# Performance work log

Hardware: AMD Instinct MI355X
Metric: run time of the kernel (lower is better)

## Reference

```python
import jax, jax.numpy as jnp
import numpy as np
import math

THETA = 10000.0

def apply_rope(x, start_pos=0):
    # x: [B, H, S, D], rotate-half RoPE
    B, H, S, D = x.shape
    pos = jnp.arange(start_pos, start_pos + S, dtype=jnp.float32)
    inv_freq = 1.0 / (THETA ** (jnp.arange(0, D, 2, dtype=jnp.float32) / D))  # [D/2]
    ang = pos[:, None] * inv_freq[None, :]  # [S, D/2]
    cos, sin = jnp.cos(ang), jnp.sin(ang)
    x1, x2 = jnp.split(x, 2, axis=-1)
    return jnp.concatenate([x1 * cos - x2 * sin, x1 * sin + x2 * cos], axis=-1)


def setup_inputs() -> dict:
    key = jax.random.key(0)
    ks = jax.random.split(key, 9)
    B, S, E, H, D = 2, 2048, 2048, 16, 128
    s = 0.02
    return {
        "x": jax.random.normal(ks[0], (B, S, E), jnp.float32),
        "W_q": jax.random.normal(ks[1], (E, H * D), jnp.float32) * s,
        "b_q": jnp.zeros((H * D,), jnp.float32),
        "W_k": jax.random.normal(ks[2], (E, D), jnp.float32) * s,
        "b_k": jnp.zeros((D,), jnp.float32),
        "W_v": jax.random.normal(ks[3], (E, D), jnp.float32) * s,
        "b_v": jnp.zeros((D,), jnp.float32),
        "W_o": jax.random.normal(ks[4], (H * D, E), jnp.float32) * s,
        "b_o": jnp.zeros((E,), jnp.float32),
    }


def reference(x, W_q, b_q, W_k, b_k, W_v, b_v, W_o, b_o):
    B, S, E = x.shape
    D = W_k.shape[1]
    H = W_q.shape[1] // D
    # projections (weights stored [in, out])
    q = (x @ W_q + b_q).reshape(B, S, H, D).transpose(0, 2, 1, 3)   # [B,H,S,D]
    k = (x @ W_k + b_k).reshape(B, S, 1, D).transpose(0, 2, 1, 3)   # [B,1,S,D]
    v = (x @ W_v + b_v).reshape(B, S, 1, D).transpose(0, 2, 1, 3)   # [B,1,S,D]
    # RoPE (cache is None -> start_pos = 0)
    q = apply_rope(q, 0)
    k = apply_rope(k, 0)
    # shared-KV attention: k head dim broadcasts over H q heads
    scores = jnp.einsum("bhqd,bokd->bhqk", q, k) / math.sqrt(D)     # [B,H,S,S]
    causal = jnp.tril(jnp.ones((S, S), dtype=bool))
    scores = jnp.where(causal, scores, -jnp.inf)
    attn = jax.nn.softmax(scores, axis=-1)
    out = jnp.einsum("bhqk,bokd->bhqd", attn, v)                    # [B,H,S,D]
    out = out.transpose(0, 2, 1, 3).reshape(B, S, H * D)
    out = out @ W_o + b_o                                           # dropout is identity in eval
    return out
```

## Files before the change

### kernel.cpp

```cpp
#include <hip/hip_runtime.h>
#include <stdint.h>

typedef __bf16 bf16x8 __attribute__((ext_vector_type(8)));
typedef __bf16 bf16x2 __attribute__((ext_vector_type(2)));
typedef float  f32x4  __attribute__((ext_vector_type(4)));
typedef short  s16x8  __attribute__((ext_vector_type(8)));

__device__ inline unsigned short f2b(float f) {
  unsigned int u = __builtin_bit_cast(unsigned int, f);
  u += 0x7FFFu + ((u >> 16) & 1u);
  return (unsigned short)(u >> 16);
}
__device__ inline float b2f(unsigned short h) {
  unsigned int u = ((unsigned int)h) << 16;
  return __builtin_bit_cast(float, u);
}
__device__ inline unsigned int pkcvt(float a, float b) {
  bf16x2 t;
  t[0] = (__bf16)a;
  t[1] = (__bf16)b;
  return __builtin_bit_cast(unsigned int, t);
}
__device__ inline void gload_lds16(const void* g, void* l) {
  __builtin_amdgcn_global_load_lds(
      (const __attribute__((address_space(1))) unsigned int*)g,
      (__attribute__((address_space(3))) unsigned int*)l, 16, 0, 0);
}

__global__ void k_cvt_bf16(const float* __restrict__ in, unsigned short* __restrict__ out, int n4) {
  int i = blockIdx.x * blockDim.x + threadIdx.x;
  if (i < n4) {
    float4 v = ((const float4*)in)[i];
    ushort4 o;
    o.x = f2b(v.x); o.y = f2b(v.y); o.z = f2b(v.z); o.w = f2b(v.w);
    ((ushort4*)out)[i] = o;
  }
}

__global__ void k_transpose(const float* __restrict__ Wq, const float* __restrict__ Wk,
                            const float* __restrict__ Wv, const float* __restrict__ Wo,
                            unsigned short* __restrict__ dstQKV, unsigned short* __restrict__ dstO) {
  __shared__ float tile[32][33];
  int n0 = blockIdx.x * 32;
  int k0 = blockIdx.y * 32;
  const float* src; int ldn, noff, K;
  unsigned short* dst;
  if (blockIdx.z == 0) {
    K = 2048; dst = dstQKV;
    if (n0 < 2048)       { src = Wq; ldn = 2048; noff = n0; }
    else if (n0 < 2176)  { src = Wk; ldn = 128;  noff = n0 - 2048; }
    else                 { src = Wv; ldn = 128;  noff = n0 - 2176; }
  } else {
    if (n0 >= 2048) return;
    K = 2048; dst = dstO;
    src = Wo; ldn = 2048; noff = n0;
  }
  int tx = threadIdx.x & 31, ty = threadIdx.x >> 5;
  for (int yy = ty; yy < 32; yy += 8)
    tile[yy][tx] = src[(size_t)(k0 + yy) * ldn + noff + tx];
  __syncthreads();
  for (int yy = ty; yy < 32; yy += 8)
    dst[(size_t)(n0 + yy) * K + k0 + tx] = f2b(tile[tx][yy]);
}

__global__ void k_bias_concat(const float* __restrict__ bq, const float* __restrict__ bk,
                              const float* __restrict__ bv, float* __restrict__ dst) {
  int i = blockIdx.x * 256 + threadIdx.x;
  if (i < 2304) dst[i] = (i < 2048) ? bq[i] : (i < 2176 ? bk[i - 2048] : bv[i - 2176]);
}

template<int OUT_BF16>
__global__ __launch_bounds__(256)
void k_gemm_lds(const unsigned short* __restrict__ A, const unsigned short* __restrict__ Bt,
                const float* __restrict__ bias, void* __restrict__ Cout,
                int M, int N, int K) {
  __shared__ unsigned short As[2][4096];
  __shared__ unsigned short Bs[2][4096];
  const int tid  = threadIdx.x;
  const int lane = tid & 63, wid = tid >> 6;
  const int lr = lane & 15, lk = lane >> 4;
  const int wr = wid >> 1,  wc = wid & 1;
  const int mb = blockIdx.y * 128, nb = blockIdx.x * 128;

  const int srow = tid >> 2, scb = (tid & 3) * 8;
  const size_t gA = (size_t)(mb + srow) * K + scb;
  const size_t gB = (size_t)(nb + srow) * K + scb;
  const int ldso = wid * 512;

  f32x4 acc[4][4];
  #pragma unroll
  for (int i = 0; i < 4; ++i)
    #pragma unroll
    for (int j = 0; j < 4; ++j) acc[i][j] = (f32x4){0.f, 0.f, 0.f, 0.f};

  auto stage = [&](int buf, int kt) {
    const size_t ko = (size_t)kt * 32;
    gload_lds16(A  + gA + ko,                  &As[buf][ldso]);
    gload_lds16(A  + gA + 64 * (size_t)K + ko, &As[buf][2048 + ldso]);
    gload_lds16(Bt + gB + ko,                  &Bs[buf][ldso]);
    gload_lds16(Bt + gB + 64 * (size_t)K + ko, &Bs[buf][2048 + ldso]);
  };

  const int ktn = K >> 5;
  stage(0, 0);

  int cur = 0;
  #pragma unroll 1
  for (int kt = 0; kt < ktn; ++kt) {
    if (kt + 1 < ktn) {
      stage(cur ^ 1, kt + 1);
      asm volatile("s_waitcnt vmcnt(4)" ::: "memory");
    } else {
      asm volatile("s_waitcnt vmcnt(0)" ::: "memory");
    }
    __builtin_amdgcn_sched_barrier(0);
    __builtin_amdgcn_s_barrier();
    bf16x8 af[4], bfv[4];
    #pragma unroll
    for (int m = 0; m < 4; ++m)
      af[m]  = *(const bf16x8*)&As[cur][(wr * 64 + m * 16 + lr) * 32 + lk * 8];
    #pragma unroll
    for (int n = 0; n < 4; ++n)
      bfv[n] = *(const bf16x8*)&Bs[cur][(wc * 64 + n * 16 + lr) * 32 + lk * 8];
    #pragma unroll
    for (int m = 0; m < 4; ++m)
      #pragma unroll
      for (int n = 0; n < 4; ++n)
        acc[m][n] = __builtin_amdgcn_mfma_f32_16x16x32_bf16(af[m], bfv[n], acc[m][n], 0, 0, 0);
    __builtin_amdgcn_s_barrier();
    cur ^= 1;
  }

  const int r0 = mb + wr * 64, c0 = nb + wc * 64;
  #pragma unroll
  for (int m = 0; m < 4; ++m) {
    #pragma unroll
    for (int n = 0; n < 4; ++n) {
      int col = c0 + n * 16 + lr;
      float bb = bias[col];
      #pragma unroll
      for (int r = 0; r < 4; ++r) {
        int row = r0 + m * 16 + lk * 4 + r;
        float v = acc[m][n][r] + bb;
        if (OUT_BF16) ((unsigned short*)Cout)[(size_t)row * N + col] = f2b(v);
        else          ((float*)Cout)[(size_t)row * N + col] = v;
      }
    }
  }
}

__global__ void k_rope(const unsigned short* __restrict__ qkv,
                       unsigned short* __restrict__ qr,
                       unsigned short* __restrict__ kr,
                       int S, int H) {
  int R = blockIdx.x * 4 + (threadIdx.x >> 6);
  int lane = threadIdx.x & 63;
  int per_b = S * (H + 1);
  int b = R / per_b;
  int rem = R - b * per_b;
  int s = rem / (H + 1);
  int j = rem - s * (H + 1);
  const unsigned short* src = qkv + (size_t)(b * S + s) * 2304 + (j < H ? j * 128 : 2048);
  float x1 = b2f(src[lane]);
  float x2 = b2f(src[lane + 64]);
  float invf = expf(-(float)lane * (9.210340371976184f / 64.0f));
  float ang = (float)s * invf;
  float c = cosf(ang), sn = sinf(ang);
  float o1 = x1 * c - x2 * sn;
  float o2 = x1 * sn + x2 * c;
  unsigned short* dst;
  if (j < H) {
    const float scale = 0.08838834764831845f;
    o1 *= scale; o2 *= scale;
    dst = qr + ((size_t)(b * H + j) * S + s) * 128;
  } else {
    dst = kr + ((size_t)(b * S) + s) * 128;
  }
  dst[lane]      = f2b(o1);
  dst[lane + 64] = f2b(o2);
}

__global__ void k_vtrans(const unsigned short* __restrict__ qkv,
                         unsigned short* __restrict__ vt, int S) {
  __shared__ unsigned short tile[32][33];
  int b = blockIdx.z;
  int s0 = blockIdx.x * 32, d0 = blockIdx.y * 32;
  int tx = threadIdx.x & 31, ty = threadIdx.x >> 5;
  for (int yy = ty; yy < 32; yy += 8)
    tile[yy][tx] = qkv[(size_t)(b * S + s0 + yy) * 2304 + 2176 + d0 + tx];
  __syncthreads();
  for (int yy = ty; yy < 32; yy += 8)
    vt[((size_t)b * 128 + d0 + yy) * S + s0 + tx] = tile[tx][yy];
}

__global__ __launch_bounds__(256)
void k_attn(const unsigned short* __restrict__ qr,
            const unsigned short* __restrict__ kr,
            const unsigned short* __restrict__ vt,
            unsigned short* __restrict__ attn_out,
            int S, int H) {
  const int b = blockIdx.z, h = blockIdx.y;
  const int tid = threadIdx.x, wid = tid >> 6, lane = tid & 63;
  const int lr = lane & 15, lk = lane >> 4;

  __shared__ unsigned short Kt[2][64 * 128];
  __shared__ unsigned short Vt[2][128 * 64];
  __shared__ unsigned short P_all[4][16][72];
  unsigned short (*P)[72] = P_all[wid];

  const char* kbyte = (const char*)(kr + (size_t)b * S * 128);
  const char* vbyte = (const char*)(vt + (size_t)b * 128 * S);
  const size_t vrow_bytes = (size_t)S * 2;

  const int krow0 = tid >> 4;
  const int kcb   = (tid & 15) << 4;
  const int vd0   = tid >> 3;
  const int vcb   = (tid & 7) << 4;
  const int lds_woff = (wid * 1024) >> 1;

  const int ksw = (lr & 7) << 4;

  const int ntiles = gridDim.x * 2;

  #pragma unroll 1
  for (int half = 0; half < 2; ++half) {
    const int qt  = (half == 0) ? blockIdx.x : (ntiles - 1 - blockIdx.x);
    const int qb0 = qt * 64;
    const int qw  = qb0 + wid * 16;

    const unsigned short* qptr = qr + ((size_t)(b * H + h) * S + (qw + lr)) * 128;
    bf16x8 aq[4];
    #pragma unroll
    for (int kk = 0; kk < 4; ++kk) aq[kk] = *(const bf16x8*)(qptr + kk * 32 + lk * 8);

    f32x4 accO[8];
    #pragma unroll
    for (int t = 0; t < 8; ++t) accO[t] = (f32x4){0.f, 0.f, 0.f, 0.f};
    float lsum = 0.f;

    auto stage = [&](int buf, int kb) {
      const char* kg = kbyte + (size_t)kb * 256;
      #pragma unroll
      for (int r = 0; r < 4; ++r) {
        int row = krow0 + r * 16;
        const char* src = kg + row * 256 + (kcb ^ ((row & 7) << 4));
        gload_lds16(src, (void*)(&Kt[buf][0] + lds_woff + r * 2048));
      }
      const char* vg = vbyte + (size_t)kb * 2;
      #pragma unroll
      for (int r = 0; r < 4; ++r) {
        int d = vd0 + r * 32;
        const char* src = vg + (size_t)d * vrow_bytes + (vcb ^ ((d & 7) << 4));
        gload_lds16(src, (void*)(&Vt[buf][0] + lds_woff + r * 2048));
      }
    };

    int cur = 0;
    stage(0, 0);

    #pragma unroll 1
    for (int kb = 0; kb <= qb0; kb += 64) {
      if (kb + 64 <= qb0) {
        stage(cur ^ 1, kb + 64);
        asm volatile("s_waitcnt vmcnt(8)" ::: "memory");
      } else {
        asm volatile("s_waitcnt vmcnt(0)" ::: "memory");
      }
      __builtin_amdgcn_sched_barrier(0);
      __builtin_amdgcn_s_barrier();
      const bool diag = (kb == qb0);
      const unsigned short* Kc = &Kt[cur][0];
      const unsigned short* Vc = &Vt[cur][0];

      bf16x8 kf[4][4];
      #pragma unroll
      for (int m = 0; m < 4; ++m) {
        const char* kl = (const char*)(Kc + (m * 16 + lr) * 128);
        #pragma unroll
        for (int kk = 0; kk < 4; ++kk)
          kf[m][kk] = *(const bf16x8*)(kl + ((kk * 64 + lk * 16) ^ ksw));
      }
      f32x4 s4[4];
      #pragma unroll
      for (int m = 0; m < 4; ++m) s4[m] = (f32x4){0.f, 0.f, 0.f, 0.f};
      __builtin_amdgcn_s_setprio(1);
      #pragma unroll
      for (int kk = 0; kk < 4; ++kk)
        #pragma unroll
        for (int m = 0; m < 4; ++m)
          s4[m] = __builtin_amdgcn_mfma_f32_16x16x32_bf16(kf[m][kk], aq[kk], s4[m], 0, 0, 0);
      __builtin_amdgcn_s_setprio(0);

      #pragma unroll
      for (int m = 0; m < 4; ++m) {
        float p[4];
        #pragma unroll
        for (int r = 0; r < 4; ++r) {
          float v = __expf(s4[m][r]);
          if (diag && (m * 16 + lk * 4 + r) > (wid * 16 + lr)) v = 0.f;
          p[r] = v;
          lsum += v;
        }
        uint2 w;
        w.x = pkcvt(p[0], p[1]);
        w.y = pkcvt(p[2], p[3]);
        *(uint2*)&P[lr][m * 16 + lk * 4] = w;
      }

      #pragma unroll
      for (int ks = 0; ks < 2; ++ks) {
        bf16x8 pa = *(const bf16x8*)&P[lr][ks * 32 + lk * 8];
        __builtin_amdgcn_s_setprio(1);
        #pragma unroll
        for (int t = 0; t < 8; ++t) {
          const char* vl = (const char*)(Vc + (t * 16 + lr) * 64);
          bf16x8 bv = *(const bf16x8*)(vl + ((ks * 64 + lk * 16) ^ ksw));
          accO[t] = __builtin_amdgcn_mfma_f32_16x16x32_bf16(pa, bv, accO[t], 0, 0, 0);
        }
        __builtin_amdgcn_s_setprio(0);
      }
      __builtin_amdgcn_s_barrier();
      cur ^= 1;
    }

    lsum += __shfl_xor(lsum, 16);
    lsum += __shfl_xor(lsum, 32);
    float rl[4];
    #pragma unroll
    for (int r = 0; r < 4; ++r) rl[r] = 1.0f / __shfl(lsum, lk * 4 + r);
    #pragma unroll
    for (int t = 0; t < 8; ++t) {
      #pragma unroll
      for (int r = 0; r < 4; ++r) {
        int srow = qw + lk * 4 + r;
        float o = accO[t][r] * rl[r];
        attn_out[((size_t)(b * S) + srow) * 2048 + h * 128 + t * 16 + lr] = f2b(o);
      }
    }
  }
}

extern "C" void kernel_launch(void* const* d_in, const int* in_sizes, int n_in,
                              void* d_out, int out_size, void* d_ws, size_t ws_size,
                              hipStream_t stream) {
  const float* x  = (const float*)d_in[0];
  const float* Wq = (const float*)d_in[1];
  const float* bq = (const float*)d_in[2];
  const float* Wk = (const float*)d_in[3];
  const float* bk = (const float*)d_in[4];
  const float* Wv = (const float*)d_in[5];
  const float* bv = (const float*)d_in[6];
  const float* Wo = (const float*)d_in[7];
  const float* bo = (const float*)d_in[8];

  const int B = 2, S = 2048, E = 2048, H = 16, D = 128;
  const int M = B * S;
  const int Nqkv = H * D + 2 * D;

  char* w = (char*)d_ws;
  unsigned short* xb    = (unsigned short*)w;
  unsigned short* WqkvT = (unsigned short*)(w + 16777216);
  unsigned short* qkv   = (unsigned short*)(w + 16777216 + 9437184);
  unsigned short* qr    = (unsigned short*)(w + 16777216 + 9437184 + 18874368);
  unsigned short* kr    = qr + (size_t)B * H * S * D;
  unsigned short* vtb   = kr + (size_t)B * S * D;
  float*          cbias = (float*)(vtb + (size_t)B * S * D);
  unsigned short* WoT   = (unsigned short*)(cbias + 4096);
  unsigned short* attn_out = xb;

  k_cvt_bf16<<<dim3((M * E / 4) / 256), 256, 0, stream>>>(x, xb, M * E / 4);
  k_transpose<<<dim3(Nqkv / 32, E / 32, 2), 256, 0, stream>>>(Wq, Wk, Wv, Wo, WqkvT, WoT);
  k_bias_concat<<<dim3(9), 256, 0, stream>>>(bq, bk, bv, cbias);
  k_gemm_lds<1><<<dim3(Nqkv / 128, M / 128), 256, 0, stream>>>(xb, WqkvT, cbias, (void*)qkv, M, Nqkv, E);
  k_rope<<<dim3(B * S * (H + 1) / 4), 256, 0, stream>>>(qkv, qr, kr, S, H);
  k_vtrans<<<dim3(S / 32, D / 32, B), 256, 0, stream>>>(qkv, vtb, S);
  k_attn<<<dim3(S / 128, H, B), 256, 0, stream>>>(qr, kr, vtb, attn_out, S, H);
  k_gemm_lds<0><<<dim3(E / 128, M / 128), 256, 0, stream>>>(attn_out, WoT, bo, (void*)d_out, M, E, H * D);
}
```

Before: 208.6 us.

## Share K/V tiles across two heads per block and keep P in registers

The attention kernel now runs 512-thread blocks that each process one 64-row query tile for two heads, so every staged K/V tile in LDS is reused by eight waves instead of four. The paired query-tile scheme is replaced by one tile per block, with reversed ordering on one batch to balance causal work. K rows are permuted so the MFMA output layout of the scores directly forms the A operand for the PV product. This removes the per-wave P round trip through LDS. Swizzle patterns change to match, and the larger block raises register and occupancy pressure.

```diff
diff --git a/kernel.cpp b/kernel.cpp
--- a/kernel.cpp
+++ b/kernel.cpp
@@ -193,149 +193,145 @@
     vt[((size_t)b * 128 + d0 + yy) * S + s0 + tx] = tile[tx][yy];
 }
 
-__global__ __launch_bounds__(256)
+__global__ __launch_bounds__(512, 4)
 void k_attn(const unsigned short* __restrict__ qr,
             const unsigned short* __restrict__ kr,
             const unsigned short* __restrict__ vt,
             unsigned short* __restrict__ attn_out,
             int S, int H) {
-  const int b = blockIdx.z, h = blockIdx.y;
+  const int b = blockIdx.z;
+  const int nqt = gridDim.x;
+  const int qt = blockIdx.z ? (int)blockIdx.x : (nqt - 1 - (int)blockIdx.x);
+  const int qb0 = qt * 64;
   const int tid = threadIdx.x, wid = tid >> 6, lane = tid & 63;
   const int lr = lane & 15, lk = lane >> 4;
+  const int hh = wid >> 2, w4 = wid & 3;
+  const int h = blockIdx.y * 2 + hh;
+  const int qw = qb0 + w4 * 16;
 
   __shared__ unsigned short Kt[2][64 * 128];
   __shared__ unsigned short Vt[2][128 * 64];
-  __shared__ unsigned short P_all[4][16][72];
-  unsigned short (*P)[72] = P_all[wid];
 
   const char* kbyte = (const char*)(kr + (size_t)b * S * 128);
   const char* vbyte = (const char*)(vt + (size_t)b * 128 * S);
   const size_t vrow_bytes = (size_t)S * 2;
 
-  const int krow0 = tid >> 4;
-  const int kcb   = (tid & 15) << 4;
-  const int vd0   = tid >> 3;
-  const int vcb   = (tid & 7) << 4;
-  const int lds_woff = (wid * 1024) >> 1;
-
-  const int ksw = (lr & 7) << 4;
-
-  const int ntiles = gridDim.x * 2;
+  const unsigned short* qptr = qr + ((size_t)(b * H + h) * S + (qw + lr)) * 128;
+  bf16x8 aq[4];
+  #pragma unroll
+  for (int kk = 0; kk < 4; ++kk) aq[kk] = *(const bf16x8*)(qptr + kk * 32 + lk * 8);
+
+  f32x4 accO[8];
+  #pragma unroll
+  for (int t = 0; t < 8; ++t) accO[t] = (f32x4){0.f, 0.f, 0.f, 0.f};
+  float lsum = 0.f;
+
+  const int vsw = ((lr & 3) | ((lr >> 1) & 4)) << 4;
+
+  auto stage = [&](int buf, int kb) {
+    const char* kg = kbyte + (size_t)kb * 256;
+    #pragma unroll
+    for (int r = 0; r < 2; ++r) {
+      int row = (tid >> 4) + r * 32;
+      int sw = ((row & 3) | ((row >> 1) & 4)) << 4;
+      const char* src = kg + row * 256 + (((tid & 15) << 4) ^ sw);
+      gload_lds16(src, (void*)((char*)&Kt[buf][0] + (wid * 4 + r * 32) * 256));
+    }
+    const char* vg = vbyte + (size_t)kb * 2;
+    #pragma unroll
+    for (int r = 0; r < 2; ++r) {
+      int d = (tid >> 3) + r * 64;
+      int sw = ((d & 3) | ((d >> 1) & 4)) << 4;
+      const char* src = vg + (size_t)d * vrow_bytes + (((tid & 7) << 4) ^ sw);
+      gload_lds16(src, (void*)((char*)&Vt[buf][0] + (wid * 8 + r * 64) * 128));
+    }
+  };
+
+  int cur = 0;
+  stage(0, 0);
 
   #pragma unroll 1
-  for (int half = 0; half < 2; ++half) {
-    const int qt  = (half == 0) ? blockIdx.x : (ntiles - 1 - blockIdx.x);
-    const int qb0 = qt * 64;
-    const int qw  = qb0 + wid * 16;
-
-    const unsigned short* qptr = qr + ((size_t)(b * H + h) * S + (qw + lr)) * 128;
-    bf16x8 aq[4];
-    #pragma unroll
-    for (int kk = 0; kk < 4; ++kk) aq[kk] = *(const bf16x8*)(qptr + kk * 32 + lk * 8);
-
-    f32x4 accO[8];
-    #pragma unroll
-    for (int t = 0; t < 8; ++t) accO[t] = (f32x4){0.f, 0.f, 0.f, 0.f};
-    float lsum = 0.f;
-
-    auto stage = [&](int buf, int kb) {
-      const char* kg = kbyte + (size_t)kb * 256;
+  for (int kb = 0; kb <= qb0; kb += 64) {
+    if (kb + 64 <= qb0) {
+      stage(cur ^ 1, kb + 64);
+      asm volatile("s_waitcnt vmcnt(4)" ::: "memory");
+    } else {
+      asm volatile("s_waitcnt vmcnt(0)" ::: "memory");
+    }
+    __builtin_amdgcn_sched_barrier(0);
+    __builtin_amdgcn_s_barrier();
+    const bool diag = (kb == qb0);
+    const unsigned short* Kc = &Kt[cur][0];
+    const unsigned short* Vc = &Vt[cur][0];
+
+    bf16x8 kf[4][4];
+    #pragma unroll
+    for (int m = 0; m < 4; ++m) {
+      const int row = ((m >> 1) << 5) + ((m & 1) << 2) + ((lr >> 2) << 3) + (lr & 3);
+      const int sw = ((row & 3) | ((row >> 1) & 4)) << 4;
+      const char* kl = (const char*)Kc + row * 256;
+      #pragma unroll
+      for (int kk = 0; kk < 4; ++kk)
+        kf[m][kk] = *(const bf16x8*)(kl + ((kk * 64 + lk * 16) ^ sw));
+    }
+    f32x4 s4[4];
+    #pragma unroll
+    for (int m = 0; m < 4; ++m) s4[m] = (f32x4){0.f, 0.f, 0.f, 0.f};
+    __builtin_amdgcn_s_setprio(1);
+    #pragma unroll
+    for (int kk = 0; kk < 4; ++kk)
+      #pragma unroll
+      for (int m = 0; m < 4; ++m)
+        s4[m] = __builtin_amdgcn_mfma_f32_16x16x32_bf16(kf[m][kk], aq[kk], s4[m], 0, 0, 0);
+    __builtin_amdgcn_s_setprio(0);
+
+    uint2 pk[4];
+    #pragma unroll
+    for (int m = 0; m < 4; ++m) {
+      const int kbase = ((m >> 1) << 5) + ((m & 1) << 2) + lk * 8;
+      float p[4];
       #pragma unroll
       for (int r = 0; r < 4; ++r) {
-        int row = krow0 + r * 16;
-        const char* src = kg + row * 256 + (kcb ^ ((row & 7) << 4));
-        gload_lds16(src, (void*)(&Kt[buf][0] + lds_woff + r * 2048));
+        float v = __expf(s4[m][r]);
+        if (diag && (kbase + r) > (w4 * 16 + lr)) v = 0.f;
+        p[r] = v;
+        lsum += v;
       }
-      const char* vg = vbyte + (size_t)kb * 2;
-      #pragma unroll
-      for (int r = 0; r < 4; ++r) {
-        int d = vd0 + r * 32;
-        const char* src = vg + (size_t)d * vrow_bytes + (vcb ^ ((d & 7) << 4));
-        gload_lds16(src, (void*)(&Vt[buf][0] + lds_woff + r * 2048));
-      }
-    };
-
-    int cur = 0;
-    stage(0, 0);
-
-    #pragma unroll 1
-    for (int kb = 0; kb <= qb0; kb += 64) {
-      if (kb + 64 <= qb0) {
-        stage(cur ^ 1, kb + 64);
-        asm volatile("s_waitcnt vmcnt(8)" ::: "memory");
-      } else {
-        asm volatile("s_waitcnt vmcnt(0)" ::: "memory");
-      }
-      __builtin_amdgcn_sched_barrier(0);
-      __builtin_amdgcn_s_barrier();
-      const bool diag = (kb == qb0);
-      const unsigned short* Kc = &Kt[cur][0];
-      const unsigned short* Vc = &Vt[cur][0];
-
-      bf16x8 kf[4][4];
-      #pragma unroll
-      for (int m = 0; m < 4; ++m) {
-        const char* kl = (const char*)(Kc + (m * 16 + lr) * 128);
-        #pragma unroll
-        for (int kk = 0; kk < 4; ++kk)
-          kf[m][kk] = *(const bf16x8*)(kl + ((kk * 64 + lk * 16) ^ ksw));
-      }
-      f32x4 s4[4];
-      #pragma unroll
-      for (int m = 0; m < 4; ++m) s4[m] = (f32x4){0.f, 0.f, 0.f, 0.f};
-      __builtin_amdgcn_s_setprio(1);
-      #pragma unroll
-      for (int kk = 0; kk < 4; ++kk)
-        #pragma unroll
-        for (int m = 0; m < 4; ++m)
-          s4[m] = __builtin_amdgcn_mfma_f32_16x16x32_bf16(kf[m][kk], aq[kk], s4[m], 0, 0, 0);
-      __builtin_amdgcn_s_setprio(0);
-
-      #pragma unroll
-      for (int m = 0; m < 4; ++m) {
-        float p[4];
-        #pragma unroll
-        for (int r = 0; r < 4; ++r) {
-          float v = __expf(s4[m][r]);
-          if (diag && (m * 16 + lk * 4 + r) > (wid * 16 + lr)) v = 0.f;
-          p[r] = v;
-          lsum += v;
-        }
-        uint2 w;
-        w.x = pkcvt(p[0], p[1]);
-        w.y = pkcvt(p[2], p[3]);
-        *(uint2*)&P[lr][m * 16 + lk * 4] = w;
-      }
-
-      #pragma unroll
-      for (int ks = 0; ks < 2; ++ks) {
-        bf16x8 pa = *(const bf16x8*)&P[lr][ks * 32 + lk * 8];
-        __builtin_amdgcn_s_setprio(1);
-        #pragma unroll
-        for (int t = 0; t < 8; ++t) {
-          const char* vl = (const char*)(Vc + (t * 16 + lr) * 64);
-          bf16x8 bv = *(const bf16x8*)(vl + ((ks * 64 + lk * 16) ^ ksw));
-          accO[t] = __builtin_amdgcn_mfma_f32_16x16x32_bf16(pa, bv, accO[t], 0, 0, 0);
-        }
-        __builtin_amdgcn_s_setprio(0);
-      }
-      __builtin_amdgcn_s_barrier();
-      cur ^= 1;
-    }
-
-    lsum += __shfl_xor(lsum, 16);
-    lsum += __shfl_xor(lsum, 32);
-    float rl[4];
-    #pragma unroll
-    for (int r = 0; r < 4; ++r) rl[r] = 1.0f / __shfl(lsum, lk * 4 + r);
+      pk[m].x = pkcvt(p[0], p[1]);
+      pk[m].y = pkcvt(p[2], p[3]);
+    }
+    uint4 ua, ub;
+    ua.x = pk[0].x; ua.y = pk[0].y; ua.z = pk[1].x; ua.w = pk[1].y;
+    ub.x = pk[2].x; ub.y = pk[2].y; ub.z = pk[3].x; ub.w = pk[3].y;
+    bf16x8 pa0 = __builtin_bit_cast(bf16x8, ua);
+    bf16x8 pa1 = __builtin_bit_cast(bf16x8, ub);
+
+    __builtin_amdgcn_s_setprio(1);
     #pragma unroll
     for (int t = 0; t < 8; ++t) {
-      #pragma unroll
-      for (int r = 0; r < 4; ++r) {
-        int srow = qw + lk * 4 + r;
-        float o = accO[t][r] * rl[r];
-        attn_out[((size_t)(b * S) + srow) * 2048 + h * 128 + t * 16 + lr] = f2b(o);
-      }
+      const char* vl = (const char*)(Vc + (t * 16 + lr) * 64);
+      bf16x8 bv0 = *(const bf16x8*)(vl + ((lk * 16) ^ vsw));
+      accO[t] = __builtin_amdgcn_mfma_f32_16x16x32_bf16(pa0, bv0, accO[t], 0, 0, 0);
+      bf16x8 bv1 = *(const bf16x8*)(vl + ((64 + lk * 16) ^ vsw));
+      accO[t] = __builtin_amdgcn_mfma_f32_16x16x32_bf16(pa1, bv1, accO[t], 0, 0, 0);
+    }
+    __builtin_amdgcn_s_setprio(0);
+    __builtin_amdgcn_s_barrier();
+    cur ^= 1;
+  }
+
+  lsum += __shfl_xor(lsum, 16);
+  lsum += __shfl_xor(lsum, 32);
+  float rl[4];
+  #pragma unroll
+  for (int r = 0; r < 4; ++r) rl[r] = 1.0f / __shfl(lsum, lk * 4 + r);
+  #pragma unroll
+  for (int t = 0; t < 8; ++t) {
+    #pragma unroll
+    for (int r = 0; r < 4; ++r) {
+      int srow = qw + lk * 4 + r;
+      float o = accO[t][r] * rl[r];
+      attn_out[((size_t)(b * S) + srow) * 2048 + h * 128 + t * 16 + lr] = f2b(o);
     }
   }
 }
@@ -374,6 +370,6 @@
   k_gemm_lds<1><<<dim3(Nqkv / 128, M / 128), 256, 0, stream>>>(xb, WqkvT, cbias, (void*)qkv, M, Nqkv, E);
   k_rope<<<dim3(B * S * (H + 1) / 4), 256, 0, stream>>>(qkv, qr, kr, S, H);
   k_vtrans<<<dim3(S / 32, D / 32, B), 256, 0, stream>>>(qkv, vtb, S);
-  k_attn<<<dim3(S / 128, H, B), 256, 0, stream>>>(qr, kr, vtb, attn_out, S, H);
+  k_attn<<<dim3(S / 64, H / 2, B), 512, 0, stream>>>(qr, kr, vtb, attn_out, S, H);
   k_gemm_lds<0><<<dim3(E / 128, M / 128), 256, 0, stream>>>(attn_out, WoT, bo, (void*)d_out, M, E, H * D);
 }
```

After: 214.5 us. 2.8% more time.

## Rewrite projection GEMMs as 8-wave 128x256 tiles with triple-buffered swizzled LDS

Applied to the files above, without the earlier changes.

Replaces the 4-wave 128x128 GEMM with a 512-thread kernel computing 128x256 tiles at a K step of 64. A three-stage LDS ring prefetches two steps ahead, and the prefetch loads are spread across four MFMA phases, with s_setprio raised around the MFMA bursts. LDS rows are XOR-swizzled to avoid bank conflicts on fragment reads. This aims to hide global-load latency and raise MFMA utilisation, at the cost of 144KB of LDS (one block per CU) and fewer blocks for the QKV GEMM, whose N of 2304 divides into only 9 column tiles.

```diff
diff --git a/kernel.cpp b/kernel.cpp
--- a/kernel.cpp
+++ b/kernel.cpp
@@ -70,22 +70,21 @@
 }
 
 template<int OUT_BF16>
-__global__ __launch_bounds__(256)
-void k_gemm_lds(const unsigned short* __restrict__ A, const unsigned short* __restrict__ Bt,
-                const float* __restrict__ bias, void* __restrict__ Cout,
-                int M, int N, int K) {
-  __shared__ unsigned short As[2][4096];
-  __shared__ unsigned short Bs[2][4096];
-  const int tid  = threadIdx.x;
-  const int lane = tid & 63, wid = tid >> 6;
+__global__ __launch_bounds__(512)
+void k_gemm8(const unsigned short* __restrict__ A, const unsigned short* __restrict__ Bt,
+             const float* __restrict__ bias, void* __restrict__ Cout,
+             int M, int N, int K) {
+  __shared__ __align__(16) char smem[3][49152];
+  const int tid = threadIdx.x, lane = tid & 63, wid = tid >> 6;
   const int lr = lane & 15, lk = lane >> 4;
-  const int wr = wid >> 1,  wc = wid & 1;
-  const int mb = blockIdx.y * 128, nb = blockIdx.x * 128;
-
-  const int srow = tid >> 2, scb = (tid & 3) * 8;
-  const size_t gA = (size_t)(mb + srow) * K + scb;
-  const size_t gB = (size_t)(nb + srow) * K + scb;
-  const int ldso = wid * 512;
+  const int wr = wid >> 2, wc = wid & 3;
+  const int mb = blockIdx.y * 128, nb = blockIdx.x * 256;
+
+  const char* Ab = (const char*)A;
+  const char* Bb = (const char*)Bt;
+  const int srow8 = lane >> 3;
+  const int scolb = (((lane & 7) << 4) ^ ((srow8 & 7) << 4));
+  const int fsw = (lr & 7) << 4;
 
   f32x4 acc[4][4];
   #pragma unroll
@@ -93,42 +92,71 @@
     #pragma unroll
     for (int j = 0; j < 4; ++j) acc[i][j] = (f32x4){0.f, 0.f, 0.f, 0.f};
 
-  auto stage = [&](int buf, int kt) {
-    const size_t ko = (size_t)kt * 32;
-    gload_lds16(A  + gA + ko,                  &As[buf][ldso]);
-    gload_lds16(A  + gA + 64 * (size_t)K + ko, &As[buf][2048 + ldso]);
-    gload_lds16(Bt + gB + ko,                  &Bs[buf][ldso]);
-    gload_lds16(Bt + gB + 64 * (size_t)K + ko, &Bs[buf][2048 + ldso]);
+  auto stageA = [&](int buf, int kt) {
+    #pragma unroll
+    for (int r = 0; r < 2; ++r) {
+      int row = r * 64 + wid * 8 + srow8;
+      const char* src = Ab + ((size_t)(mb + row) * K + kt * 64) * 2 + scolb;
+      gload_lds16(src, &smem[buf][r * 8192 + wid * 1024]);
+    }
   };
-
-  const int ktn = K >> 5;
-  stage(0, 0);
+  auto stageBr = [&](int buf, int kt, int r) {
+    int row = r * 64 + wid * 8 + srow8;
+    const char* src = Bb + ((size_t)(nb + row) * K + kt * 64) * 2 + scolb;
+    gload_lds16(src, &smem[buf][16384 + r * 8192 + wid * 1024]);
+  };
+
+  const int ktn = K >> 6;
+  stageA(0, 0);
+  #pragma unroll
+  for (int r = 0; r < 4; ++r) stageBr(0, 0, r);
+  stageA(1, 1);
+  #pragma unroll
+  for (int r = 0; r < 4; ++r) stageBr(1, 1, r);
 
   int cur = 0;
   #pragma unroll 1
   for (int kt = 0; kt < ktn; ++kt) {
-    if (kt + 1 < ktn) {
-      stage(cur ^ 1, kt + 1);
-      asm volatile("s_waitcnt vmcnt(4)" ::: "memory");
-    } else {
-      asm volatile("s_waitcnt vmcnt(0)" ::: "memory");
-    }
+    const char* Ac = smem[cur];
+    const char* Bc = smem[cur] + 16384;
+    const bool pf = (kt + 2 < ktn);
+    const int nbuf = (cur + 2 >= 3) ? cur - 1 : cur + 2;
+    if (kt + 1 < ktn) asm volatile("s_waitcnt vmcnt(6)" ::: "memory");
+    else              asm volatile("s_waitcnt vmcnt(0)" ::: "memory");
     __builtin_amdgcn_sched_barrier(0);
     __builtin_amdgcn_s_barrier();
-    bf16x8 af[4], bfv[4];
-    #pragma unroll
-    for (int m = 0; m < 4; ++m)
-      af[m]  = *(const bf16x8*)&As[cur][(wr * 64 + m * 16 + lr) * 32 + lk * 8];
-    #pragma unroll
-    for (int n = 0; n < 4; ++n)
-      bfv[n] = *(const bf16x8*)&Bs[cur][(wc * 64 + n * 16 + lr) * 32 + lk * 8];
-    #pragma unroll
-    for (int m = 0; m < 4; ++m)
-      #pragma unroll
-      for (int n = 0; n < 4; ++n)
-        acc[m][n] = __builtin_amdgcn_mfma_f32_16x16x32_bf16(af[m], bfv[n], acc[m][n], 0, 0, 0);
-    __builtin_amdgcn_s_barrier();
-    cur ^= 1;
+
+    bf16x8 af[4][2];
+    #pragma unroll
+    for (int ph = 0; ph < 4; ++ph) {
+      if (ph == 0) {
+        #pragma unroll
+        for (int m = 0; m < 4; ++m) {
+          const char* ab = Ac + (wr * 64 + m * 16 + lr) * 128;
+          af[m][0] = *(const bf16x8*)(ab + ((lk * 16) ^ fsw));
+          af[m][1] = *(const bf16x8*)(ab + ((64 + lk * 16) ^ fsw));
+        }
+      }
+      const char* bbp = Bc + (wc * 64 + ph * 16 + lr) * 128;
+      bf16x8 bf0 = *(const bf16x8*)(bbp + ((lk * 16) ^ fsw));
+      bf16x8 bf1 = *(const bf16x8*)(bbp + ((64 + lk * 16) ^ fsw));
+      if (pf) {
+        if (ph == 0) stageA(nbuf, kt + 2);
+        else if (ph == 1) { stageBr(nbuf, kt + 2, 0); stageBr(nbuf, kt + 2, 1); }
+        else if (ph == 2) stageBr(nbuf, kt + 2, 2);
+        else              stageBr(nbuf, kt + 2, 3);
+      }
+      __builtin_amdgcn_s_barrier();
+      __builtin_amdgcn_s_setprio(1);
+      #pragma unroll
+      for (int m = 0; m < 4; ++m) {
+        acc[m][ph] = __builtin_amdgcn_mfma_f32_16x16x32_bf16(af[m][0], bf0, acc[m][ph], 0, 0, 0);
+        acc[m][ph] = __builtin_amdgcn_mfma_f32_16x16x32_bf16(af[m][1], bf1, acc[m][ph], 0, 0, 0);
+      }
+      __builtin_amdgcn_s_setprio(0);
+      __builtin_amdgcn_s_barrier();
+    }
+    cur = (cur + 1 == 3) ? 0 : cur + 1;
   }
 
   const int r0 = mb + wr * 64, c0 = nb + wc * 64;
@@ -139,9 +167,9 @@
       int col = c0 + n * 16 + lr;
       float bb = bias[col];
       #pragma unroll
-      for (int r = 0; r < 4; ++r) {
-        int row = r0 + m * 16 + lk * 4 + r;
-        float v = acc[m][n][r] + bb;
+      for (int rr = 0; rr < 4; ++rr) {
+        int row = r0 + m * 16 + lk * 4 + rr;
+        float v = acc[m][n][rr] + bb;
         if (OUT_BF16) ((unsigned short*)Cout)[(size_t)row * N + col] = f2b(v);
         else          ((float*)Cout)[(size_t)row * N + col] = v;
       }
@@ -371,9 +399,9 @@
   k_cvt_bf16<<<dim3((M * E / 4) / 256), 256, 0, stream>>>(x, xb, M * E / 4);
   k_transpose<<<dim3(Nqkv / 32, E / 32, 2), 256, 0, stream>>>(Wq, Wk, Wv, Wo, WqkvT, WoT);
   k_bias_concat<<<dim3(9), 256, 0, stream>>>(bq, bk, bv, cbias);
-  k_gemm_lds<1><<<dim3(Nqkv / 128, M / 128), 256, 0, stream>>>(xb, WqkvT, cbias, (void*)qkv, M, Nqkv, E);
+  k_gemm8<1><<<dim3(Nqkv / 256, M / 128), 512, 0, stream>>>(xb, WqkvT, cbias, (void*)qkv, M, Nqkv, E);
   k_rope<<<dim3(B * S * (H + 1) / 4), 256, 0, stream>>>(qkv, qr, kr, S, H);
   k_vtrans<<<dim3(S / 32, D / 32, B), 256, 0, stream>>>(qkv, vtb, S);
   k_attn<<<dim3(S / 128, H, B), 256, 0, stream>>>(qr, kr, vtb, attn_out, S, H);
-  k_gemm_lds<0><<<dim3(E / 128, M / 128), 256, 0, stream>>>(attn_out, WoT, bo, (void*)d_out, M, E, H * D);
-}
+  k_gemm8<0><<<dim3(E / 256, M / 128), 512, 0, stream>>>(attn_out, WoT, bo, (void*)d_out, M, E, H * D);
+}
```

New measurement: 214.9 us. 1.03x slower.

## Triple-buffer GEMM loads, swizzle block order, fold bias concat into epilogue

Applied to the files above, without the earlier changes.

The projection GEMM now keeps three LDS stages and prefetches two K-tiles ahead, waiting on older loads with deeper vmcnt counts, to hide more global-load latency. Workgroup indices are remapped with a stride-8 swizzle to change which tiles run concurrently and improve L2 reuse. The separate bias-concatenation kernel is removed; the QKV GEMM epilogue selects among the three bias arrays directly, saving one launch. The extra stage raises LDS use per block, which may reduce occupancy.

```diff
diff --git a/kernel.cpp b/kernel.cpp
--- a/kernel.cpp
+++ b/kernel.cpp
@@ -63,24 +63,24 @@
     dst[(size_t)(n0 + yy) * K + k0 + tx] = f2b(tile[tx][yy]);
 }
 
-__global__ void k_bias_concat(const float* __restrict__ bq, const float* __restrict__ bk,
-                              const float* __restrict__ bv, float* __restrict__ dst) {
-  int i = blockIdx.x * 256 + threadIdx.x;
-  if (i < 2304) dst[i] = (i < 2048) ? bq[i] : (i < 2176 ? bk[i - 2048] : bv[i - 2176]);
-}
-
-template<int OUT_BF16>
+template<int OUT_BF16, int BIAS3>
 __global__ __launch_bounds__(256)
 void k_gemm_lds(const unsigned short* __restrict__ A, const unsigned short* __restrict__ Bt,
-                const float* __restrict__ bias, void* __restrict__ Cout,
+                const float* __restrict__ b0, const float* __restrict__ b1,
+                const float* __restrict__ b2, void* __restrict__ Cout,
                 int M, int N, int K) {
-  __shared__ unsigned short As[2][4096];
-  __shared__ unsigned short Bs[2][4096];
+  __shared__ unsigned short As[3][4096];
+  __shared__ unsigned short Bs[3][4096];
   const int tid  = threadIdx.x;
   const int lane = tid & 63, wid = tid >> 6;
   const int lr = lane & 15, lk = lane >> 4;
   const int wr = wid >> 1,  wc = wid & 1;
-  const int mb = blockIdx.y * 128, nb = blockIdx.x * 128;
+
+  const int nwg = gridDim.x * gridDim.y;
+  const int flat = blockIdx.y * gridDim.x + blockIdx.x;
+  const int swz = (flat & 7) * (nwg >> 3) + (flat >> 3);
+  const int mb = (swz / gridDim.x) * 128;
+  const int nb = (swz % gridDim.x) * 128;
 
   const int srow = tid >> 2, scb = (tid & 3) * 8;
   const size_t gA = (size_t)(mb + srow) * K + scb;
@@ -103,12 +103,16 @@
 
   const int ktn = K >> 5;
   stage(0, 0);
+  stage(1, 1);
 
   int cur = 0;
   #pragma unroll 1
   for (int kt = 0; kt < ktn; ++kt) {
-    if (kt + 1 < ktn) {
-      stage(cur ^ 1, kt + 1);
+    if (kt + 2 < ktn) {
+      int nbuf = cur + 2; if (nbuf >= 3) nbuf -= 3;
+      stage(nbuf, kt + 2);
+      asm volatile("s_waitcnt vmcnt(8)" ::: "memory");
+    } else if (kt + 1 < ktn) {
       asm volatile("s_waitcnt vmcnt(4)" ::: "memory");
     } else {
       asm volatile("s_waitcnt vmcnt(0)" ::: "memory");
@@ -128,7 +132,7 @@
       for (int n = 0; n < 4; ++n)
         acc[m][n] = __builtin_amdgcn_mfma_f32_16x16x32_bf16(af[m], bfv[n], acc[m][n], 0, 0, 0);
     __builtin_amdgcn_s_barrier();
-    cur ^= 1;
+    ++cur; if (cur == 3) cur = 0;
   }
 
   const int r0 = mb + wr * 64, c0 = nb + wc * 64;
@@ -137,7 +141,9 @@
     #pragma unroll
     for (int n = 0; n < 4; ++n) {
       int col = c0 + n * 16 + lr;
-      float bb = bias[col];
+      float bb;
+      if (BIAS3) bb = (col < 2048) ? b0[col] : (col < 2176 ? b1[col - 2048] : b2[col - 2176]);
+      else       bb = b0[col];
       #pragma unroll
       for (int r = 0; r < 4; ++r) {
         int row = r0 + m * 16 + lk * 4 + r;
@@ -370,10 +376,9 @@
 
   k_cvt_bf16<<<dim3((M * E / 4) / 256), 256, 0, stream>>>(x, xb, M * E / 4);
   k_transpose<<<dim3(Nqkv / 32, E / 32, 2), 256, 0, stream>>>(Wq, Wk, Wv, Wo, WqkvT, WoT);
-  k_bias_concat<<<dim3(9), 256, 0, stream>>>(bq, bk, bv, cbias);
-  k_gemm_lds<1><<<dim3(Nqkv / 128, M / 128), 256, 0, stream>>>(xb, WqkvT, cbias, (void*)qkv, M, Nqkv, E);
+  k_gemm_lds<1, 1><<<dim3(Nqkv / 128, M / 128), 256, 0, stream>>>(xb, WqkvT, bq, bk, bv, (void*)qkv, M, Nqkv, E);
   k_rope<<<dim3(B * S * (H + 1) / 4), 256, 0, stream>>>(qkv, qr, kr, S, H);
   k_vtrans<<<dim3(S / 32, D / 32, B), 256, 0, stream>>>(qkv, vtb, S);
   k_attn<<<dim3(S / 128, H, B), 256, 0, stream>>>(qr, kr, vtb, attn_out, S, H);
-  k_gemm_lds<0><<<dim3(E / 128, M / 128), 256, 0, stream>>>(attn_out, WoT, bo, (void*)d_out, M, E, H * D);
-}
+  k_gemm_lds<0, 0><<<dim3(E / 128, M / 128), 256, 0, stream>>>(attn_out, WoT, bo, nullptr, nullptr, (void*)d_out, M, E, H * D);
+}
```

Measured after the change: 204.3 us. -2.1%, faster.
